# Kernel optimization log

Measured on AMD Instinct MI355X. Metric: run time of the kernel, lower is better.

## Reference

```python
import jax, jax.numpy as jnp
import numpy as np

A, H, HI = 4, 3, 2  # nagents, n_pol_heads, n_intr_rew_heads (sep_extr_head=True)
# leave-one-out index table: row i lists all agents k != i, in ascending order (torch loop order)
LOO = np.array([[k for k in range(A) if k != i] for i in range(A)])  # [A, A-1]


def setup_inputs() -> dict:
    key = jax.random.key(0)
    ks = jax.random.split(key, 12)
    B, S, C, D = 32768, 256, 16, 128  # batch, vect_state_size, action_size, hidden_dim
    IN = C * (A - 1) + D  # 176 critic input dim
    r = lambda k, shp, s=0.05: jax.random.normal(k, shp, dtype=jnp.float32) * s
    return {
        "state_vect": jax.random.normal(ks[0], (B, S), dtype=jnp.float32),
        "acs": jax.random.normal(ks[1], (A, H, B, C), dtype=jnp.float32),
        "enc_W": r(ks[2], (S, D)),
        "enc_b": r(ks[3], (D,)),
        "extr_W1": r(ks[4], (H, A, IN, D)),
        "extr_b1": r(ks[5], (H, A, D)),
        "extr_W2": r(ks[6], (H, A, D, C)),
        "extr_b2": r(ks[7], (H, A, C)),
        "intr_W1": r(ks[8], (HI, A, IN, D)),
        "intr_b1": r(ks[9], (HI, A, D)),
        "intr_W2": r(ks[10], (HI, A, D, C)),
        "intr_b2": r(ks[11], (HI, A, C)),
    }


def reference(state_vect, acs, enc_W, enc_b, extr_W1, extr_b1, extr_W2, extr_b2,
              intr_W1, intr_b1, intr_W2, intr_b2):
    B, C = acs.shape[2], acs.shape[3]
    D = enc_W.shape[1]
    # shared state encoder: Linear -> ReLU
    enc = jax.nn.relu(state_vect @ enc_W + enc_b)  # [B, D]
    # leave-one-out action concat per (agent, head): cat(acs[k!=i, j]) ++ enc
    rel = acs[LOO]                                 # [A, A-1, H, B, C]
    rel = rel.transpose(0, 2, 3, 1, 4).reshape(A, H, B, (A - 1) * C)
    x = jnp.concatenate([rel, jnp.broadcast_to(enc, (A, H, B, D))], axis=-1)  # [A,H,B,IN]
    # greedy action index of agent i's own head-j policy output
    int_acs = jnp.argmax(acs, axis=-1)             # [A, H, B]

    def critic(xin, W1, b1, W2, b2):
        # xin: [A, Hc, B, IN]; W1: [Hc, A, IN, D]; W2: [Hc, A, D, C]
        h = jax.nn.relu(jnp.einsum('ahbi,haid->ahbd', xin, W1)
                        + b1.transpose(1, 0, 2)[:, :, None, :])
        return (jnp.einsum('ahbd,hadc->ahbc', h, W2)
                + b2.transpose(1, 0, 2)[:, :, None, :])  # [A, Hc, B, C]

    extr_all_q = critic(x, extr_W1, extr_b1, extr_W2, extr_b2)          # [A,H,B,C]
    extr_q = jnp.take_along_axis(extr_all_q, int_acs[..., None], axis=-1)  # [A,H,B,1]
    # intr critics exist only for heads j>=1 (sep_extr_head=True -> offset -1)
    intr_all_q = critic(x[:, 1:], intr_W1, intr_b1, intr_W2, intr_b2)   # [A,HI,B,C]
    intr_q = jnp.take_along_axis(intr_all_q, int_acs[:, 1:, :, None], axis=-1)  # [A,HI,B,1]
    return extr_q, intr_q
```

## Files before the change

### kernel.cpp

```cpp
#include <hip/hip_runtime.h>

#define NA 4
#define NH 3
#define NHI 2
#define Bsz 32768
#define Ssz 256
#define Csz 16
#define Dsz 128
#define INsz 176
#define NP 20
#define KP 192

typedef __bf16 v8bf __attribute__((ext_vector_type(8)));
typedef float v4f __attribute__((ext_vector_type(4)));

#define OFF_ENC    0
#define OFF_ACSBF  8388608
#define OFF_W1F    20971520
#define OFF_W2T    22020096
#define OFF_AMX    22102016
#define OFF_ZERO   22495232

#define N_ACSROW (NA*NH*Bsz)
#define N_W1F   (NP*192*32)
#define N_W2T   (NP*Csz*Dsz)
#define N_ZERO  16
#define N_PREP  (N_ACSROW+N_W1F+N_W2T+N_ZERO)
#define ENC_BLOCKS (Bsz / 64)
#define PREP_BLOCKS ((N_PREP + 255) / 256)

__global__ __launch_bounds__(256) void pe_kernel(
    const float* __restrict__ sv, const float* __restrict__ encb,
    const float* __restrict__ acs, const float* __restrict__ encW,
    const float* __restrict__ eW1, const float* __restrict__ iW1,
    const float* __restrict__ eW2, const float* __restrict__ iW2,
    char* __restrict__ ws)
{
    __shared__ __bf16 encs[8 * 8 * 512];
    const int t = threadIdx.x;

    if (blockIdx.x < ENC_BLOCKS) {
        #pragma unroll
        for (int i = 0; i < 16; ++i) {
            const int slot = i * 256 + t;
            const int kcnt = slot >> 6;
            const int ln   = slot & 63;
            const int kc = kcnt >> 3, nt = kcnt & 7;
            const int qq = ln >> 4, mm = ln & 15;
            const int krow = kc * 32 + qq * 8;
            const int col  = nt * 16 + mm;
            v8bf o;
            #pragma unroll
            for (int j = 0; j < 8; ++j)
                o[j] = (__bf16)encW[(size_t)(krow + j) * Dsz + col];
            *(v8bf*)&encs[(size_t)kcnt * 512 + ln * 8] = o;
        }
        __syncthreads();

        const int wv = t >> 6, lane = t & 63, m = lane & 15, q = lane >> 4;
        const int R = blockIdx.x * 64 + wv * 16 + m;
        __bf16* enc = (__bf16*)(ws + OFF_ENC);

        v4f acc[8];
        #pragma unroll
        for (int nt = 0; nt < 8; ++nt) acc[nt] = (v4f){0.f, 0.f, 0.f, 0.f};

        const float* arow = sv + (size_t)R * Ssz + q * 8;
        #pragma unroll
        for (int kc = 0; kc < 8; ++kc) {
            float4 f0 = *(const float4*)(arow + kc * 32);
            float4 f1 = *(const float4*)(arow + kc * 32 + 4);
            v8bf af;
            af[0]=(__bf16)f0.x; af[1]=(__bf16)f0.y; af[2]=(__bf16)f0.z; af[3]=(__bf16)f0.w;
            af[4]=(__bf16)f1.x; af[5]=(__bf16)f1.y; af[6]=(__bf16)f1.z; af[7]=(__bf16)f1.w;
            #pragma unroll
            for (int nt = 0; nt < 8; ++nt) {
                v8bf bf = *(const v8bf*)&encs[((size_t)kc * 8 + nt) * 512 + lane * 8];
                acc[nt] = __builtin_amdgcn_mfma_f32_16x16x32_bf16(af, bf, acc[nt], 0, 0, 0);
            }
        }
        const int rbase = blockIdx.x * 64 + wv * 16 + q * 4;
        #pragma unroll
        for (int nt = 0; nt < 8; ++nt) {
            const float bias = encb[nt * 16 + m];
            #pragma unroll
            for (int rg = 0; rg < 4; ++rg) {
                float v = acc[nt][rg] + bias;
                v = v > 0.f ? v : 0.f;
                enc[(size_t)(rbase + rg) * Dsz + nt * 16 + m] = (__bf16)v;
            }
        }
        return;
    }

    long tid = (long)(blockIdx.x - ENC_BLOCKS) * 256 + t;

    if (tid < N_ACSROW) {
        const float4* src = (const float4*)(acs + (size_t)tid * 16);
        float4 f0 = src[0], f1 = src[1], f2 = src[2], f3 = src[3];
        float v[16] = {f0.x,f0.y,f0.z,f0.w, f1.x,f1.y,f1.z,f1.w,
                       f2.x,f2.y,f2.z,f2.w, f3.x,f3.y,f3.z,f3.w};
        v8bf o0, o1;
        #pragma unroll
        for (int i = 0; i < 8; ++i) { o0[i] = (__bf16)v[i]; o1[i] = (__bf16)v[8 + i]; }
        v8bf* dst = (v8bf*)(ws + OFF_ACSBF) + tid * 2;
        dst[0] = o0; dst[1] = o1;
        float best = v[0]; int bi = 0;
        #pragma unroll
        for (int c = 1; c < 16; ++c) if (v[c] > best) { best = v[c]; bi = c; }
        ((unsigned char*)(ws + OFF_AMX))[tid] = (unsigned char)bi;
        return;
    }
    tid -= N_ACSROW;
    if (tid < N_W1F) {
        const int n4 = (int)(tid & 31) * 4;
        const int k  = (int)((tid >> 5) % 192);
        const int p  = (int)(tid / 6144);
        const float* W1;
        if (p < 12) { int ai = p / 3, hj = p % 3; W1 = eW1 + (size_t)(hj * NA + ai) * INsz * Dsz; }
        else { int qq = p - 12; int ai = qq >> 1, jj = qq & 1; W1 = iW1 + (size_t)(jj * NA + ai) * INsz * Dsz; }
        float4 f = (k < INsz) ? *(const float4*)(W1 + (size_t)k * Dsz + n4)
                              : (float4){0.f, 0.f, 0.f, 0.f};
        const int kc = k >> 5, q = (k >> 3) & 3, j = k & 7;
        __bf16* dst = (__bf16*)(ws + OFF_W1F);
        const float fv[4] = {f.x, f.y, f.z, f.w};
        #pragma unroll
        for (int i = 0; i < 4; ++i) {
            const int n = n4 + i, nt = n >> 4, m = n & 15;
            dst[((size_t)(p * 6 + kc) * 8 + nt) * 512 + (q * 16 + m) * 8 + j] = (__bf16)fv[i];
        }
        return;
    }
    tid -= N_W1F;
    if (tid < N_W2T) {
        int d = (int)(tid & 127);
        int rest = (int)(tid >> 7);
        int c = rest & 15, p = rest >> 4;
        const float* W2;
        if (p < 12) { int ai = p / 3, hj = p % 3; W2 = eW2 + (size_t)(hj * NA + ai) * Dsz * Csz; }
        else { int qq = p - 12; int ai = qq >> 1, jj = qq & 1; W2 = iW2 + (size_t)(jj * NA + ai) * Dsz * Csz; }
        ((__bf16*)(ws + OFF_W2T))[(size_t)p * Csz * Dsz + (size_t)c * Dsz + d] = (__bf16)W2[(size_t)d * Csz + c];
        return;
    }
    tid -= N_W2T;
    if (tid < N_ZERO) ((float*)(ws + OFF_ZERO))[tid] = 0.f;
}

__global__ __launch_bounds__(256, 2) void critic_kernel(
    const float* __restrict__ eb1, const float* __restrict__ eb2,
    const float* __restrict__ ib1, const float* __restrict__ ib2,
    const char* __restrict__ ws, float* __restrict__ out)
{
    __shared__ __bf16 w1s[6 * 8 * 512];

    const int t = threadIdx.x;
    const int p  = blockIdx.y;
    const int rb = blockIdx.x;
    const int wv = t >> 6, lane = t & 63, m = lane & 15, q = lane >> 4;
    const int rw = rb * 256 + wv * 64;

    int ai, hj;
    const float *b1, *b2;
    float* outp;
    if (p < 12) {
        ai = p / 3; hj = p % 3;
        const int wi = hj * NA + ai;
        b1 = eb1 + (size_t)wi * Dsz; b2 = eb2 + (size_t)wi * Csz;
        outp = out + (size_t)(ai * NH + hj) * Bsz;
    } else {
        const int qq = p - 12; ai = qq >> 1; const int jj = qq & 1; hj = jj + 1;
        const int wi = jj * NA + ai;
        b1 = ib1 + (size_t)wi * Dsz; b2 = ib2 + (size_t)wi * Csz;
        outp = out + (size_t)NA * NH * Bsz + (size_t)(ai * NHI + jj) * Bsz;
    }

    const __bf16* acsb = (const __bf16*)(ws + OFF_ACSBF);
    const __bf16* encp = (const __bf16*)(ws + OFF_ENC);
    const __bf16* w1f  = (const __bf16*)(ws + OFF_W1F) + (size_t)p * 6 * 8 * 512;
    const __bf16* w2t  = (const __bf16*)(ws + OFF_W2T) + (size_t)p * Csz * Dsz;
    const unsigned char* amx = (const unsigned char*)(ws + OFF_AMX) + (size_t)(ai * NH + hj) * Bsz + rw;
    const __bf16* zerop = (const __bf16*)(ws + OFF_ZERO);

    {
        const v8bf* src = (const v8bf*)w1f;
        v8bf* dst = (v8bf*)w1s;
        #pragma unroll
        for (int i = 0; i < 12; ++i)
            dst[i * 256 + t] = src[i * 256 + t];
    }

    const int loo0 = 0 + (0 >= ai), loo1 = 1 + (1 >= ai), loo2 = 2 + (2 >= ai);
    const __bf16* a0p = acsb + (size_t)(loo0 * NH + hj) * Bsz * Csz;
    const __bf16* a1p = acsb + (size_t)(loo1 * NH + hj) * Bsz * Csz;
    const __bf16* a2p = acsb + (size_t)(loo2 * NH + hj) * Bsz * Csz;

    const int R0 = rw + m;
    const __bf16* base[6];
    int strd[6];
    base[0] = (q < 2) ? (a0p + (size_t)R0 * Csz + q * 8) : (a1p + (size_t)R0 * Csz + (q - 2) * 8);
    strd[0] = Csz;
    base[1] = (q < 2) ? (a2p + (size_t)R0 * Csz + q * 8) : (encp + (size_t)R0 * Dsz + (q - 2) * 8);
    strd[1] = (q < 2) ? Csz : Dsz;
    base[2] = encp + (size_t)R0 * Dsz + 16 + q * 8;  strd[2] = Dsz;
    base[3] = encp + (size_t)R0 * Dsz + 48 + q * 8;  strd[3] = Dsz;
    base[4] = encp + (size_t)R0 * Dsz + 80 + q * 8;  strd[4] = Dsz;
    base[5] = (q < 2) ? (encp + (size_t)R0 * Dsz + 112 + q * 8) : zerop;
    strd[5] = (q < 2) ? Dsz : 0;

    v4f acc[4][8];
    #pragma unroll
    for (int i = 0; i < 4; ++i)
        #pragma unroll
        for (int j = 0; j < 8; ++j)
            acc[i][j] = (v4f){0.f, 0.f, 0.f, 0.f};

    __syncthreads();

    #pragma unroll
    for (int kc = 0; kc < 6; ++kc) {
        v8bf af[4];
        #pragma unroll
        for (int mt = 0; mt < 4; ++mt)
            af[mt] = *(const v8bf*)(base[kc] + (size_t)(mt * 16) * strd[kc]);
        #pragma unroll
        for (int nt = 0; nt < 8; ++nt) {
            v8bf bf = *(const v8bf*)&w1s[((size_t)kc * 8 + nt) * 512 + lane * 8];
            #pragma unroll
            for (int mt = 0; mt < 4; ++mt)
                acc[mt][nt] = __builtin_amdgcn_mfma_f32_16x16x32_bf16(af[mt], bf, acc[mt][nt], 0, 0, 0);
        }
    }

    float b1v[8];
    #pragma unroll
    for (int nt = 0; nt < 8; ++nt) b1v[nt] = b1[nt * 16 + m];

    #pragma unroll
    for (int mt = 0; mt < 4; ++mt) {
        const int rowb = mt * 16 + q * 4;
        const unsigned int cw = *(const unsigned int*)(amx + rowb);
        #pragma unroll
        for (int rg = 0; rg < 4; ++rg) {
            const int c = (cw >> (8 * rg)) & 255;
            const __bf16* wc = w2t + (size_t)c * Dsz + m;
            float partial = 0.f;
            #pragma unroll
            for (int nt = 0; nt < 8; ++nt) {
                float h = acc[mt][nt][rg] + b1v[nt];
                h = h > 0.f ? h : 0.f;
                partial += h * (float)wc[nt * 16];
            }
            partial += __shfl_xor(partial, 1, 64);
            partial += __shfl_xor(partial, 2, 64);
            partial += __shfl_xor(partial, 4, 64);
            partial += __shfl_xor(partial, 8, 64);
            if (m == 0)
                outp[rw + rowb + rg] = partial + b2[c];
        }
    }
}

extern "C" void kernel_launch(void* const* d_in, const int* in_sizes, int n_in,
                              void* d_out, int out_size, void* d_ws, size_t ws_size,
                              hipStream_t stream) {
    const float* sv   = (const float*)d_in[0];
    const float* acs  = (const float*)d_in[1];
    const float* encW = (const float*)d_in[2];
    const float* encb = (const float*)d_in[3];
    const float* eW1  = (const float*)d_in[4];
    const float* eb1  = (const float*)d_in[5];
    const float* eW2  = (const float*)d_in[6];
    const float* eb2  = (const float*)d_in[7];
    const float* iW1  = (const float*)d_in[8];
    const float* ib1  = (const float*)d_in[9];
    const float* iW2  = (const float*)d_in[10];
    const float* ib2  = (const float*)d_in[11];
    float* out = (float*)d_out;
    char* ws = (char*)d_ws;

    hipLaunchKernelGGL(pe_kernel, dim3(ENC_BLOCKS + PREP_BLOCKS), dim3(256), 0, stream,
                       sv, encb, acs, encW, eW1, iW1, eW2, iW2, ws);
    hipLaunchKernelGGL(critic_kernel, dim3(Bsz / 256, NP), dim3(256), 0, stream,
                       eb1, eb2, ib1, ib2, ws, out);
}
```

Measured before the change: 183.9 us.

## Pipeline critic A-fragment loads, stage W2/biases in LDS, and batch encoder rows

The critic kernel now double-buffers its A-operand loads, fetching the next K-chunk's fragments while the current chunk's MFMAs run. It also stages W2, b1 and b2 in shared memory and prefetches the argmax bytes before the GEMM, so the epilogue's gathers hit LDS instead of global memory. Separately, the encoder part of the prep kernel uses fewer blocks (128), each looping over 4 row groups, so the bf16 encW conversion into LDS is paid once per 256 rows instead of once per 64. The cost is more registers in the critic, which could hurt occupancy under launch_bounds(256,2), and less parallelism in the encoder phase.

Result: no change. 184.5 us (+0.3%).

```diff
diff --git a/kernel.cpp b/kernel.cpp
--- a/kernel.cpp
+++ b/kernel.cpp
@@ -26,7 +26,7 @@
 #define N_W2T   (NP*Csz*Dsz)
 #define N_ZERO  16
 #define N_PREP  (N_ACSROW+N_W1F+N_W2T+N_ZERO)
-#define ENC_BLOCKS (Bsz / 64)
+#define ENC_BLOCKS 128
 #define PREP_BLOCKS ((N_PREP + 255) / 256)
 
 __global__ __launch_bounds__(256) void pe_kernel(
@@ -58,36 +58,39 @@
         __syncthreads();
 
         const int wv = t >> 6, lane = t & 63, m = lane & 15, q = lane >> 4;
-        const int R = blockIdx.x * 64 + wv * 16 + m;
         __bf16* enc = (__bf16*)(ws + OFF_ENC);
 
-        v4f acc[8];
-        #pragma unroll
-        for (int nt = 0; nt < 8; ++nt) acc[nt] = (v4f){0.f, 0.f, 0.f, 0.f};
-
-        const float* arow = sv + (size_t)R * Ssz + q * 8;
-        #pragma unroll
-        for (int kc = 0; kc < 8; ++kc) {
-            float4 f0 = *(const float4*)(arow + kc * 32);
-            float4 f1 = *(const float4*)(arow + kc * 32 + 4);
-            v8bf af;
-            af[0]=(__bf16)f0.x; af[1]=(__bf16)f0.y; af[2]=(__bf16)f0.z; af[3]=(__bf16)f0.w;
-            af[4]=(__bf16)f1.x; af[5]=(__bf16)f1.y; af[6]=(__bf16)f1.z; af[7]=(__bf16)f1.w;
+        for (int it = 0; it < 4; ++it) {
+            const int R = blockIdx.x * 256 + it * 64 + wv * 16 + m;
+
+            v4f acc[8];
+            #pragma unroll
+            for (int nt = 0; nt < 8; ++nt) acc[nt] = (v4f){0.f, 0.f, 0.f, 0.f};
+
+            const float* arow = sv + (size_t)R * Ssz + q * 8;
+            #pragma unroll
+            for (int kc = 0; kc < 8; ++kc) {
+                float4 f0 = *(const float4*)(arow + kc * 32);
+                float4 f1 = *(const float4*)(arow + kc * 32 + 4);
+                v8bf af;
+                af[0]=(__bf16)f0.x; af[1]=(__bf16)f0.y; af[2]=(__bf16)f0.z; af[3]=(__bf16)f0.w;
+                af[4]=(__bf16)f1.x; af[5]=(__bf16)f1.y; af[6]=(__bf16)f1.z; af[7]=(__bf16)f1.w;
+                #pragma unroll
+                for (int nt = 0; nt < 8; ++nt) {
+                    v8bf bf = *(const v8bf*)&encs[((size_t)kc * 8 + nt) * 512 + lane * 8];
+                    acc[nt] = __builtin_amdgcn_mfma_f32_16x16x32_bf16(af, bf, acc[nt], 0, 0, 0);
+                }
+            }
+            const int rbase = blockIdx.x * 256 + it * 64 + wv * 16 + q * 4;
             #pragma unroll
             for (int nt = 0; nt < 8; ++nt) {
-                v8bf bf = *(const v8bf*)&encs[((size_t)kc * 8 + nt) * 512 + lane * 8];
-                acc[nt] = __builtin_amdgcn_mfma_f32_16x16x32_bf16(af, bf, acc[nt], 0, 0, 0);
-            }
-        }
-        const int rbase = blockIdx.x * 64 + wv * 16 + q * 4;
-        #pragma unroll
-        for (int nt = 0; nt < 8; ++nt) {
-            const float bias = encb[nt * 16 + m];
-            #pragma unroll
-            for (int rg = 0; rg < 4; ++rg) {
-                float v = acc[nt][rg] + bias;
-                v = v > 0.f ? v : 0.f;
-                enc[(size_t)(rbase + rg) * Dsz + nt * 16 + m] = (__bf16)v;
+                const float bias = encb[nt * 16 + m];
+                #pragma unroll
+                for (int rg = 0; rg < 4; ++rg) {
+                    float v = acc[nt][rg] + bias;
+                    v = v > 0.f ? v : 0.f;
+                    enc[(size_t)(rbase + rg) * Dsz + nt * 16 + m] = (__bf16)v;
+                }
             }
         }
         return;
@@ -152,6 +155,9 @@
     const char* __restrict__ ws, float* __restrict__ out)
 {
     __shared__ __bf16 w1s[6 * 8 * 512];
+    __shared__ __bf16 w2s[16 * 128];
+    __shared__ float  b1s[128];
+    __shared__ float  b2s[16];
 
     const int t = threadIdx.x;
     const int p  = blockIdx.y;
@@ -187,6 +193,9 @@
         #pragma unroll
         for (int i = 0; i < 12; ++i)
             dst[i * 256 + t] = src[i * 256 + t];
+        ((v8bf*)w2s)[t] = ((const v8bf*)w2t)[t];
+        if (t < 128) b1s[t] = b1[t];
+        if (t < 16)  b2s[t] = b2[t];
     }
 
     const int loo0 = 0 + (0 >= ai), loo1 = 1 + (1 >= ai), loo2 = 2 + (2 >= ai);
@@ -207,6 +216,11 @@
     base[5] = (q < 2) ? (encp + (size_t)R0 * Dsz + 112 + q * 8) : zerop;
     strd[5] = (q < 2) ? Dsz : 0;
 
+    unsigned int cw4[4];
+    #pragma unroll
+    for (int mt = 0; mt < 4; ++mt)
+        cw4[mt] = *(const unsigned int*)(amx + mt * 16 + q * 4);
+
     v4f acc[4][8];
     #pragma unroll
     for (int i = 0; i < 4; ++i)
@@ -214,35 +228,43 @@
         for (int j = 0; j < 8; ++j)
             acc[i][j] = (v4f){0.f, 0.f, 0.f, 0.f};
 
+    v8bf afc[4], afn[4];
+    #pragma unroll
+    for (int mt = 0; mt < 4; ++mt)
+        afc[mt] = *(const v8bf*)(base[0] + (size_t)(mt * 16) * strd[0]);
+
     __syncthreads();
 
     #pragma unroll
     for (int kc = 0; kc < 6; ++kc) {
-        v8bf af[4];
-        #pragma unroll
-        for (int mt = 0; mt < 4; ++mt)
-            af[mt] = *(const v8bf*)(base[kc] + (size_t)(mt * 16) * strd[kc]);
+        if (kc < 5) {
+            #pragma unroll
+            for (int mt = 0; mt < 4; ++mt)
+                afn[mt] = *(const v8bf*)(base[kc + 1] + (size_t)(mt * 16) * strd[kc + 1]);
+        }
         #pragma unroll
         for (int nt = 0; nt < 8; ++nt) {
             v8bf bf = *(const v8bf*)&w1s[((size_t)kc * 8 + nt) * 512 + lane * 8];
             #pragma unroll
             for (int mt = 0; mt < 4; ++mt)
-                acc[mt][nt] = __builtin_amdgcn_mfma_f32_16x16x32_bf16(af[mt], bf, acc[mt][nt], 0, 0, 0);
-        }
+                acc[mt][nt] = __builtin_amdgcn_mfma_f32_16x16x32_bf16(afc[mt], bf, acc[mt][nt], 0, 0, 0);
+        }
+        #pragma unroll
+        for (int mt = 0; mt < 4; ++mt)
+            afc[mt] = afn[mt];
     }
 
     float b1v[8];
     #pragma unroll
-    for (int nt = 0; nt < 8; ++nt) b1v[nt] = b1[nt * 16 + m];
+    for (int nt = 0; nt < 8; ++nt) b1v[nt] = b1s[nt * 16 + m];
 
     #pragma unroll
     for (int mt = 0; mt < 4; ++mt) {
-        const int rowb = mt * 16 + q * 4;
-        const unsigned int cw = *(const unsigned int*)(amx + rowb);
+        const unsigned int cw = cw4[mt];
         #pragma unroll
         for (int rg = 0; rg < 4; ++rg) {
             const int c = (cw >> (8 * rg)) & 255;
-            const __bf16* wc = w2t + (size_t)c * Dsz + m;
+            const __bf16* wc = &w2s[c * 128 + m];
             float partial = 0.f;
             #pragma unroll
             for (int nt = 0; nt < 8; ++nt) {
@@ -255,7 +277,7 @@
             partial += __shfl_xor(partial, 4, 64);
             partial += __shfl_xor(partial, 8, 64);
             if (m == 0)
-                outp[rw + rowb + rg] = partial + b2[c];
+                outp[rw + mt * 16 + q * 4 + rg] = partial + b2s[c];
         }
     }
 }
```
